# Performance work log

Measured on AMD Instinct MI355X. Metric: run time of the kernel, lower is better.

Reference implementation:

```python
import jax, jax.numpy as jnp
import numpy as np

N, D = 8192, 1024


def setup_inputs() -> dict:
    key = jax.random.key(0)
    k1, k2, k3, k4 = jax.random.split(key, 4)
    return {
        "first_features": jax.random.normal(k1, (N, D), dtype=jnp.float32),
        "second_features": jax.random.normal(k2, (N, D), dtype=jnp.float32),
        "first_label": jax.random.randint(k3, (N,), 0, N, dtype=jnp.int64),
        "second_label": jax.random.randint(k4, (N,), 0, N, dtype=jnp.int64),
        "logit_scale": jnp.asarray(10.0, dtype=jnp.float32),
        "logit_bias": jnp.asarray(-10.0, dtype=jnp.float32),
    }


def reference(first_features, second_features, first_label, second_label,
              logit_scale, logit_bias):
    # logits: [N, N] = scale * A @ B^T + bias
    logits = logit_scale * jnp.einsum("id,jd->ij", first_features, second_features)
    logits = logits + logit_bias
    # ground truth: +1 where labels match, -1 elsewhere
    labels = jnp.where(first_label[:, None] == second_label[None, :], 1.0, -1.0)
    labels = labels.astype(logits.dtype)
    # loss = sum(-logsigmoid(labels * logits)) / N  (mask_diagonal=False)
    loss = -jnp.sum(jax.nn.log_sigmoid(labels * logits)) / first_features.shape[0]
    return loss
```

## Files before the change

### kernel.cpp

```cpp
#include <hip/hip_runtime.h>
#include <hip/hip_bf16.h>
#include <stdint.h>

#define N_TOK 8192
#define D_K   1024
#define NB    128
#define NT    16
#define GSTRIDE 32768

typedef __attribute__((ext_vector_type(4)))  int   i32x4;
typedef __attribute__((ext_vector_type(8)))  int   i32x8;
typedef __attribute__((ext_vector_type(16))) float f32x16;

__device__ __forceinline__ unsigned int f32_to_e4m3(float x) {
  uint32_t u = __builtin_bit_cast(uint32_t, x);
  unsigned int s = (u >> 24) & 0x80u;
  float ax = __builtin_fabsf(x);
  if (ax < 0.015625f) {
    int q = (int)rintf(ax * 512.0f);
    return s | (unsigned int)q;
  }
  uint32_t au = u & 0x7FFFFFFFu;
  uint32_t v = au + 0x7FFFFu + ((au >> 20) & 1u);
  int em = (int)(v >> 20) - 960;
  if (em > 0x7E) em = 0x7E;
  return s | (unsigned int)em;
}

__global__ void __launch_bounds__(256)
convert_perm_kernel(const float* __restrict__ a, const float* __restrict__ b,
                    unsigned char* __restrict__ oa,
                    unsigned char* __restrict__ ob,
                    float* __restrict__ out) {
  __shared__ unsigned int P[8192];
  const int blk = (int)blockIdx.x;
  if (blk == 0 && threadIdx.x == 0) out[0] = 0.0f;
  const int g   = blk >> 1;
  const float* __restrict__ src = (blk & 1) ? b : a;
  unsigned char* __restrict__ dst = (blk & 1) ? ob : oa;
  const int tid = threadIdx.x;

  const float4* s4 = (const float4*)src + (size_t)g * 8192;
  const int koff = (tid >> 4) * 512 + ((tid >> 3) & 1) * 256 + (tid & 7);
#pragma unroll
  for (int i = 0; i < 32; ++i) {
    float4 v = s4[i * 256 + tid];
    unsigned int w = f32_to_e4m3(v.x) | (f32_to_e4m3(v.y) << 8) |
                     (f32_to_e4m3(v.z) << 16) | (f32_to_e4m3(v.w) << 24);
    P[koff + i * 8] = w;
  }
  __syncthreads();
  i32x4* d4 = (i32x4*)(dst + (size_t)g * GSTRIDE);
  const i32x4* p4 = (const i32x4*)P;
#pragma unroll
  for (int i = 0; i < 8; ++i) d4[i * 256 + tid] = p4[i * 256 + tid];
}

__global__ void __launch_bounds__(256)
sigc_kernel(const unsigned char* __restrict__ A8,
            const unsigned char* __restrict__ B8,
            const int* __restrict__ labA, const int* __restrict__ labB,
            const float* __restrict__ scale_p, const float* __restrict__ bias_p,
            float* __restrict__ out) {
  __shared__ int sLabA[NB];
  __shared__ int sLabB[NB];
  __shared__ float sPart[4];

  const int tid  = threadIdx.x;
  const int lane = tid & 63;
  const int wid  = tid >> 6;
  const int wr   = wid >> 1;
  const int wc   = wid & 1;

  const int bid = (int)blockIdx.x;
  const int xcd = bid & 7;
  const int ii  = bid >> 3;
  const int rr  = (xcd >> 1) * 16 + (ii & 15);
  const int cc  = (xcd & 1) * 32 + (ii >> 4);

  if (tid < 128)      sLabA[tid] = labA[rr * NB + tid];
  else                sLabB[tid - 128] = labB[cc * NB + (tid - 128)];

  const unsigned char* aF[2];
  const unsigned char* bF[2];
#pragma unroll
  for (int f = 0; f < 2; ++f) {
    aF[f] = A8 + (size_t)(rr * 4 + wr * 2 + f) * GSTRIDE + lane * 32;
    bF[f] = B8 + (size_t)(cc * 4 + wc * 2 + f) * GSTRIDE + lane * 32;
  }

#define LOADT(fa, fb, T) do {                                              \
    fa[0] = *(const i32x8*)(aF[0] + (T) * 2048);                           \
    fa[1] = *(const i32x8*)(aF[1] + (T) * 2048);                           \
    fb[0] = *(const i32x8*)(bF[0] + (T) * 2048);                           \
    fb[1] = *(const i32x8*)(bF[1] + (T) * 2048);                           \
  } while (0)

#define MMAT(fa, fb) do {                                                  \
    __builtin_amdgcn_s_setprio(1);                                         \
    acc00 = __builtin_amdgcn_mfma_scale_f32_32x32x64_f8f6f4(               \
        fa[0], fb[0], acc00, 0, 0, 0, 0x7F7F7F7F, 0, 0x7F7F7F7F);          \
    acc01 = __builtin_amdgcn_mfma_scale_f32_32x32x64_f8f6f4(               \
        fa[0], fb[1], acc01, 0, 0, 0, 0x7F7F7F7F, 0, 0x7F7F7F7F);          \
    acc10 = __builtin_amdgcn_mfma_scale_f32_32x32x64_f8f6f4(               \
        fa[1], fb[0], acc10, 0, 0, 0, 0x7F7F7F7F, 0, 0x7F7F7F7F);          \
    acc11 = __builtin_amdgcn_mfma_scale_f32_32x32x64_f8f6f4(               \
        fa[1], fb[1], acc11, 0, 0, 0, 0x7F7F7F7F, 0, 0x7F7F7F7F);          \
    __builtin_amdgcn_s_setprio(0); } while (0)

  f32x16 acc00 = {0}, acc01 = {0}, acc10 = {0}, acc11 = {0};

  i32x8 fA0[2], fB0[2], fA1[2], fB1[2];

  LOADT(fA0, fB0, 0);

#pragma unroll
  for (int t2 = 0; t2 < NT / 2; ++t2) {
    const int e = 2 * t2;
    LOADT(fA1, fB1, e + 1);
    MMAT(fA0, fB0);
    if (t2 < NT / 2 - 1) LOADT(fA0, fB0, e + 2);
    MMAT(fA1, fB1);
  }

  __syncthreads();

  const float L2E = 1.4426950408889634f;
  const float sl2e = scale_p[0] * L2E;
  const float bl2e = bias_p[0] * L2E;
  const int colIn = lane & 31;
  const int hi32  = lane >> 5;
  const int colL0 = sLabB[wc * 64 + colIn];
  const int colL1 = sLabB[wc * 64 + 32 + colIn];
  int rl0[16], rl1[16];
#pragma unroll
  for (int r = 0; r < 16; ++r) {
    const int rbase = (r & 3) + 8 * (r >> 2) + 4 * hi32;
    rl0[r] = sLabA[wr * 64 + rbase];
    rl1[r] = sLabA[wr * 64 + 32 + rbase];
  }

  float S1a = 0.f, S2a = 0.f, Sma = 0.f, pa = 1.0f;
  float S1b = 0.f, S2b = 0.f, Smb = 0.f, pb = 1.0f;
  float S1c = 0.f, S2c = 0.f, Smc = 0.f, pc = 1.0f;
  float S1d = 0.f, S2d = 0.f, Smd = 0.f, pd = 1.0f;

#define EPI(ACC, RL, CL, S1x, S2x, Smx, px) do {                           \
    _Pragma("unroll") for (int _r = 0; _r < 16; ++_r) {                    \
      const float _u = fmaf(sl2e, ACC[_r], bl2e);                          \
      const float _au = fabsf(_u);                                         \
      S1x += _u;                                                           \
      S2x += _au;                                                          \
      px = fmaf(px, __builtin_amdgcn_exp2f(-_au), px);                     \
      Smx += (RL[_r] == (CL)) ? _u : 0.0f;                                 \
    } } while (0)

  EPI(acc00, rl0, colL0, S1a, S2a, Sma, pa);
  EPI(acc01, rl0, colL1, S1b, S2b, Smb, pb);
  EPI(acc10, rl1, colL0, S1c, S2c, Smc, pc);
  EPI(acc11, rl1, colL1, S1d, S2d, Smd, pd);

  const float S1 = (S1a + S1b) + (S1c + S1d);
  const float S2 = (S2a + S2b) + (S2c + S2d);
  const float Sm = (Sma + Smb) + (Smc + Smd);
  const float pp = (pa * pb) * (pc * pd);
  float loss = 0.5f * (S1 + S2) - Sm + __builtin_amdgcn_logf(pp);

#pragma unroll
  for (int off = 32; off > 0; off >>= 1) loss += __shfl_down(loss, off, 64);
  if (lane == 0) sPart[wid] = loss;
  __syncthreads();
  if (tid == 0) {
    const float s = (sPart[0] + sPart[1]) + (sPart[2] + sPart[3]);
    atomicAdd(out, s * (0.6931471805599453f / (float)N_TOK));
  }
}

extern "C" void kernel_launch(void* const* d_in, const int* in_sizes, int n_in,
                              void* d_out, int out_size, void* d_ws, size_t ws_size,
                              hipStream_t stream) {
  const float* a  = (const float*)d_in[0];
  const float* b  = (const float*)d_in[1];
  const int*   la = (const int*)d_in[2];
  const int*   lb = (const int*)d_in[3];
  const float* sc = (const float*)d_in[4];
  const float* bi = (const float*)d_in[5];
  float* out = (float*)d_out;

  unsigned char* wa = (unsigned char*)d_ws;
  unsigned char* wb = wa + (size_t)N_TOK * D_K;

  convert_perm_kernel<<<512, 256, 0, stream>>>(a, b, wa, wb, out);
  const int grid = (N_TOK / NB) * (N_TOK / NB);
  sigc_kernel<<<grid, 256, 0, stream>>>(wa, wb, la, lb, sc, bi, out);
}
```

Before: 100.9 us.

## Stage B tile through swizzled LDS with direct global-to-LDS loads

Instead of each wave loading its B fragments straight from global memory (each B fragment read by two waves), the block loads the whole 128-column B tile into 64KB of LDS in two halves using global_load_lds, with an XOR swizzle to avoid bank conflicts. Waves then read their B fragments from LDS, while A is still streamed from global. This halves global/L2 traffic for B but adds two full barriers with vmcnt(0) waits that serialize loading and compute. The 64KB LDS footprint also limits occupancy.

```diff
diff --git a/kernel.cpp b/kernel.cpp
--- a/kernel.cpp
+++ b/kernel.cpp
@@ -4,7 +4,6 @@
 
 #define N_TOK 8192
 #define D_K   1024
-#define NB    128
 #define NT    16
 #define GSTRIDE 32768
 
@@ -62,8 +61,9 @@
             const int* __restrict__ labA, const int* __restrict__ labB,
             const float* __restrict__ scale_p, const float* __restrict__ bias_p,
             float* __restrict__ out) {
-  __shared__ int sLabA[NB];
-  __shared__ int sLabB[NB];
+  __shared__ unsigned char ldsB[65536];
+  __shared__ int sLabA[128];
+  __shared__ int sLabB[128];
   __shared__ float sPart[4];
 
   const int tid  = threadIdx.x;
@@ -78,22 +78,43 @@
   const int rr  = (xcd >> 1) * 16 + (ii & 15);
   const int cc  = (xcd & 1) * 32 + (ii >> 4);
 
-  if (tid < 128)      sLabA[tid] = labA[rr * NB + tid];
-  else                sLabB[tid - 128] = labB[cc * NB + (tid - 128)];
-
-  const unsigned char* aF[2];
-  const unsigned char* bF[2];
-#pragma unroll
-  for (int f = 0; f < 2; ++f) {
-    aF[f] = A8 + (size_t)(rr * 4 + wr * 2 + f) * GSTRIDE + lane * 32;
-    bF[f] = B8 + (size_t)(cc * 4 + wc * 2 + f) * GSTRIDE + lane * 32;
-  }
-
-#define LOADT(fa, fb, T) do {                                              \
-    fa[0] = *(const i32x8*)(aF[0] + (T) * 2048);                           \
-    fa[1] = *(const i32x8*)(aF[1] + (T) * 2048);                           \
-    fb[0] = *(const i32x8*)(bF[0] + (T) * 2048);                           \
-    fb[1] = *(const i32x8*)(bF[1] + (T) * 2048);                           \
+  if (tid < 128)      sLabA[tid] = labA[rr * 128 + tid];
+  else                sLabB[tid - 128] = labB[cc * 128 + (tid - 128)];
+
+#define STAGE(P_) do {                                                     \
+    _Pragma("unroll") for (int _g = 0; _g < 4; ++_g) {                     \
+      const unsigned char* _gb =                                           \
+          B8 + (size_t)(cc * 4 + _g) * GSTRIDE + (P_) * 16384;             \
+      _Pragma("unroll") for (int _r = 0; _r < 4; ++_r) {                   \
+        const int _ds = _r * 256 + tid;             \
+        const int _tau = _ds >> 7;                                         \
+        const int _q   = _ds & 127;                                        \
+        const int _qs  = _q ^ ((_q >> 3) & 7);                             \
+        __builtin_amdgcn_global_load_lds(                                  \
+            (const __attribute__((address_space(1))) void*)                \
+                (_gb + _tau * 2048 + _qs * 16),                            \
+            (__attribute__((address_space(3))) void*)                      \
+                (ldsB + _g * 16384 + _r * 4096 + wid * 1024 + lane * 16),  \
+            16, 0, 0);                                                     \
+      } } } while (0)
+
+  const int swzOff0 = (lane * 32) ^ (((lane >> 2) & 7) << 4);
+  const int swzOff1 = (lane * 32 + 16) ^ (((lane >> 2) & 7) << 4);
+#define RDB(fb, TL) do {                                                   \
+    const int _b0 = (wc * 2) * 16384 + (TL) * 2048;                        \
+    const int _b1 = (wc * 2 + 1) * 16384 + (TL) * 2048;                    \
+    ((i32x4*)&fb[0])[0] = *(const i32x4*)&ldsB[_b0 + swzOff0];             \
+    ((i32x4*)&fb[0])[1] = *(const i32x4*)&ldsB[_b0 + swzOff1];             \
+    ((i32x4*)&fb[1])[0] = *(const i32x4*)&ldsB[_b1 + swzOff0];             \
+    ((i32x4*)&fb[1])[1] = *(const i32x4*)&ldsB[_b1 + swzOff1];             \
+  } while (0)
+
+  const unsigned char* aF0 =
+      A8 + (size_t)(rr * 4 + wr * 2) * GSTRIDE + lane * 32;
+  const unsigned char* aF1 = aF0 + GSTRIDE;
+#define LOADA(fa, T) do {                                                  \
+    fa[0] = *(const i32x8*)(aF0 + (T) * 2048);                             \
+    fa[1] = *(const i32x8*)(aF1 + (T) * 2048);                             \
   } while (0)
 
 #define MMAT(fa, fb) do {                                                  \
@@ -109,18 +130,38 @@
     __builtin_amdgcn_s_setprio(0); } while (0)
 
   f32x16 acc00 = {0}, acc01 = {0}, acc10 = {0}, acc11 = {0};
-
-  i32x8 fA0[2], fB0[2], fA1[2], fB1[2];
-
-  LOADT(fA0, fB0, 0);
-
-#pragma unroll
-  for (int t2 = 0; t2 < NT / 2; ++t2) {
+  i32x8 fA0[2], fA1[2], fbe[2], fbo[2];
+
+  STAGE(0);
+  asm volatile("s_waitcnt vmcnt(0)" ::: "memory");
+  __syncthreads();
+
+  LOADA(fA0, 0);
+#pragma unroll
+  for (int t2 = 0; t2 < 4; ++t2) {
     const int e = 2 * t2;
-    LOADT(fA1, fB1, e + 1);
-    MMAT(fA0, fB0);
-    if (t2 < NT / 2 - 1) LOADT(fA0, fB0, e + 2);
-    MMAT(fA1, fB1);
+    LOADA(fA1, e + 1);
+    RDB(fbe, e);
+    MMAT(fA0, fbe);
+    LOADA(fA0, e + 2);
+    RDB(fbo, e + 1);
+    MMAT(fA1, fbo);
+  }
+
+  __syncthreads();
+  STAGE(1);
+  asm volatile("s_waitcnt vmcnt(0)" ::: "memory");
+  __syncthreads();
+
+#pragma unroll
+  for (int t2 = 0; t2 < 4; ++t2) {
+    const int e = 8 + 2 * t2;
+    LOADA(fA1, e + 1);
+    RDB(fbe, e - 8);
+    MMAT(fA0, fbe);
+    if (t2 < 3) LOADA(fA0, e + 2);
+    RDB(fbo, e - 7);
+    MMAT(fA1, fbo);
   }
 
   __syncthreads();
@@ -191,6 +232,6 @@
   unsigned char* wb = wa + (size_t)N_TOK * D_K;
 
   convert_perm_kernel<<<512, 256, 0, stream>>>(a, b, wa, wb, out);
-  const int grid = (N_TOK / NB) * (N_TOK / NB);
+  const int grid = (N_TOK / 128) * (N_TOK / 128);
   sigc_kernel<<<grid, 256, 0, stream>>>(wa, wb, la, lb, sc, bi, out);
 }
```

Result: slower. 128.8 us (+27.7%).
